# Kernel optimization log

Hardware: AMD Instinct MI355X
Metric: run time of the kernel (lower is better)

The kernel has to match this reference:

```python
import jax, jax.numpy as jnp
import numpy as np

N_NODES = 20000
N_EDGES = 200000
D_MODEL = 128
N_HEADS = 8
N_LAYERS = 2  # num_gnn - 1 concat layers


def setup_inputs() -> dict:
    key = jax.random.key(0)
    ks = jax.random.split(key, 12)
    s = 0.05  # keep activations well-scaled across residual layers
    hd = D_MODEL // N_HEADS  # 16
    return {
        "x": jax.random.normal(ks[0], (N_NODES, D_MODEL), jnp.float32),
        "src": jax.random.randint(ks[1], (N_EDGES,), 0, N_NODES),
        "dst": jax.random.randint(ks[2], (N_EDGES,), 0, N_NODES),
        "Ws": jax.random.normal(ks[3], (N_LAYERS, D_MODEL, D_MODEL), jnp.float32) * s,
        "als": jax.random.normal(ks[4], (N_LAYERS, N_HEADS, hd), jnp.float32) * s,
        "ars": jax.random.normal(ks[5], (N_LAYERS, N_HEADS, hd), jnp.float32) * s,
        "bs": jax.random.normal(ks[6], (N_LAYERS, D_MODEL), jnp.float32) * s,
        "W_last": jax.random.normal(ks[7], (D_MODEL, N_HEADS * D_MODEL), jnp.float32) * s,
        "al_last": jax.random.normal(ks[8], (N_HEADS, D_MODEL), jnp.float32) * s,
        "ar_last": jax.random.normal(ks[9], (N_HEADS, D_MODEL), jnp.float32) * s,
        "b_last": jax.random.normal(ks[10], (N_HEADS * D_MODEL,), jnp.float32) * s,
    }


def gat_conv(h, src, dst, W, al, ar, b, num_nodes):
    """DGL GATConv (eval mode, dropout off): returns (N, H, D) head outputs."""
    H, D = al.shape
    feat = (h @ W).reshape(num_nodes, H, D)          # (N,H,D)
    el = jnp.sum(feat * al[None], axis=-1)           # (N,H) attn on src side
    er = jnp.sum(feat * ar[None], axis=-1)           # (N,H) attn on dst side
    e = jax.nn.leaky_relu(el[src] + er[dst], 0.2)    # (E,H)
    # edge softmax over incoming edges of each dst node, per head
    m = jax.ops.segment_max(e, dst, num_segments=num_nodes)  # (N,H)
    p = jnp.exp(e - m[dst])                          # (E,H)
    z = jax.ops.segment_sum(p, dst, num_segments=num_nodes)  # (N,H)
    a = p / z[dst]                                   # (E,H)
    msg = feat[src] * a[..., None]                   # (E,H,D) weighted messages
    rst = jax.ops.segment_sum(msg, dst, num_segments=num_nodes)  # (N,H,D)
    return rst + b.reshape(1, H, D)


def reference(x, src, dst, Ws, als, ars, bs, W_last, al_last, ar_last, b_last):
    N = x.shape[0]
    h = x
    for i in range(N_LAYERS):
        temp = gat_conv(h, src, dst, Ws[i], als[i], ars[i], bs[i], N)  # (N,H,hd)
        h = h + jax.nn.elu(temp.reshape(N, -1))       # concat heads, ELU, residual
    temp = gat_conv(h, src, dst, W_last, al_last, ar_last, b_last, N)  # (N,H,D)
    h = h + jnp.mean(temp, axis=1)                    # mean over heads, residual
    return h
```

## Files before the change

kernel.cpp:

```cpp
#include <hip/hip_runtime.h>
#include <math.h>

#define N_NODES 20000
#define N_EDGES 200000
#define DM 128
#define NH 8

typedef __attribute__((ext_vector_type(8))) short bf16x8;
typedef __attribute__((ext_vector_type(4))) float f32x4;

__device__ __forceinline__ unsigned short f2b(float f) {
  unsigned int u = __float_as_uint(f);
  unsigned int r = (u + 0x7FFFu + ((u >> 16) & 1u)) >> 16;
  return (unsigned short)r;
}
__device__ __forceinline__ float b2f(unsigned short s) {
  return __uint_as_float(((unsigned int)s) << 16);
}

__global__ __launch_bounds__(256) void degzero(int* __restrict__ deg) {
  int i = blockIdx.x * 256 + threadIdx.x;
  if (i < N_NODES) deg[i] = 0;
}

__global__ __launch_bounds__(256) void prep_all(
    const float* __restrict__ x, float* __restrict__ h, unsigned short* __restrict__ hb,
    const int* __restrict__ dstE, int* __restrict__ deg, int* __restrict__ rank,
    const float* __restrict__ Ws, unsigned short* __restrict__ wsz,
    const float* __restrict__ W_last, unsigned short* __restrict__ wpsz,
    const float* __restrict__ al_last, const float* __restrict__ ar_last,
    const float* __restrict__ b_last, unsigned short* __restrict__ wlrsz,
    float* __restrict__ mb) {
  int i = blockIdx.x * 256 + threadIdx.x;
  if (i < (N_NODES * DM) / 4) {
    float4 v = ((const float4*)x)[i];
    ((float4*)h)[i] = v;
    ((ushort4*)hb)[i] = make_ushort4(f2b(v.x), f2b(v.y), f2b(v.z), f2b(v.w));
  }
  if (i < N_EDGES) rank[i] = atomicAdd(&deg[dstE[i]], 1);
  if (i < 2 * 16384) {
    int layer = i >> 14;
    int r = i & 16383;
    int j = r & 7, l = (r >> 3) & 63, f = (r >> 9) & 7, ks = r >> 12;
    int k = ks * 32 + ((l >> 4) << 3) + j;
    int n = f * 16 + (l & 15);
    wsz[i] = f2b(Ws[(size_t)layer * 16384 + k * 128 + n]);
  }
  if (i < 131072) {
    int j = i & 7, l = (i >> 3) & 63, f = (i >> 9) & 7, ks = i >> 12;
    int k = ks * 32 + ((l >> 4) << 3) + j;
    int n = f * 16 + (l & 15);
    int h_ = k >> 7, ko = k & 127;
    wpsz[i] = f2b(W_last[(size_t)ko * 1024 + h_ * 128 + n] * 0.125f);
  }
  if (i < 2048) {
    int j = i & 7, l = (i >> 3) & 63, ks = i >> 9;
    int k = ks * 32 + ((l >> 4) << 3) + j;
    int n = l & 15;
    int hh = n & 7;
    const float* av = (n < 8) ? (al_last + hh * 128) : (ar_last + hh * 128);
    float s = 0.f;
    for (int d = 0; d < 128; ++d) s += W_last[(size_t)k * 1024 + hh * 128 + d] * av[d];
    wlrsz[i] = f2b(s);
  }
  if (i < 128) {
    float s = 0.f;
#pragma unroll
    for (int hh = 0; hh < 8; ++hh) s += b_last[hh * 128 + i];
    mb[i] = s * 0.125f;
  }
}

__global__ void scan_deg(const int* __restrict__ deg, int* __restrict__ off,
                         int* __restrict__ bbase_g, int* __restrict__ bcur_g) {
  __shared__ int part[1024];
  __shared__ int hist[16][64];
  const int tid = threadIdx.x;
  const int wv = tid >> 6, lane = tid & 63;
  const int CHUNK = (N_NODES + 1023) / 1024;
  int base = tid * CHUNK;

  for (int i = tid; i < 16 * 64; i += 1024) ((int*)hist)[i] = 0;
  __syncthreads();

  int s = 0;
  for (int i = 0; i < CHUNK; ++i) {
    int idx = base + i;
    if (idx < N_NODES) {
      int d = deg[idx];
      s += d;
      atomicAdd(&hist[wv][min(d, 63)], 1);
    }
  }
  part[tid] = s;
  __syncthreads();
  for (int ofs = 1; ofs < 1024; ofs <<= 1) {
    int v = (tid >= ofs) ? part[tid - ofs] : 0;
    __syncthreads();
    part[tid] += v;
    __syncthreads();
  }
  int run = (tid > 0) ? part[tid - 1] : 0;
  for (int i = 0; i < CHUNK; ++i) {
    int idx = base + i;
    if (idx < N_NODES) {
      off[idx] = run;
      run += deg[idx];
    }
  }
  if (tid == 0) off[N_NODES] = part[1023];

  if (wv == 0) {
    int c = 0;
#pragma unroll
    for (int w = 0; w < 16; ++w) c += hist[w][lane];
    int inc = c;
#pragma unroll
    for (int ofs = 1; ofs < 64; ofs <<= 1) {
      int v = __shfl_up(inc, ofs, 64);
      if (lane >= ofs) inc += v;
    }
    bbase_g[lane] = inc - c;
    bcur_g[lane] = 0;
  }
}

template <int K>
__device__ __forceinline__ void dev_gemm(int tile, const unsigned short* __restrict__ A,
                                         const unsigned short* __restrict__ Bsz,
                                         unsigned short* __restrict__ Cb,
                                         const float* __restrict__ al,
                                         const float* __restrict__ ar,
                                         float* __restrict__ elr, int lane, int wid) {
  const int wrow = wid & 1, wc = wid >> 1;
  const int r0 = tile * 32;
  const int arow = r0 + wrow * 16 + (lane & 15);
  const int kg = lane >> 4;

  f32x4 acc[4];
#pragma unroll
  for (int fi = 0; fi < 4; ++fi) acc[fi] = {0.f, 0.f, 0.f, 0.f};

  const bf16x8* Ap = (const bf16x8*)(A + (size_t)arow * K + kg * 8);
#pragma unroll 4
  for (int ks = 0; ks < K / 32; ++ks) {
    bf16x8 a = Ap[ks * 4];
#pragma unroll
    for (int fi = 0; fi < 4; ++fi) {
      int f = wc * 4 + fi;
      bf16x8 b = *(const bf16x8*)(Bsz + (((size_t)(ks * 8 + f) * 64 + lane) << 3));
      acc[fi] = __builtin_amdgcn_mfma_f32_16x16x32_bf16(a, b, acc[fi], 0, 0, 0);
    }
  }

  const int rbase = r0 + wrow * 16 + (lane >> 4) * 4;
#pragma unroll
  for (int fi = 0; fi < 4; ++fi) {
    int col = wc * 64 + fi * 16 + (lane & 15);
#pragma unroll
    for (int r = 0; r < 4; ++r) {
      Cb[(size_t)(rbase + r) * DM + col] = f2b(acc[fi][r]);
    }
  }

#pragma unroll
  for (int fi = 0; fi < 4; ++fi) {
    int hh = wc * 4 + fi;
    float alv = al[hh * 16 + (lane & 15)];
    float arv = ar[hh * 16 + (lane & 15)];
#pragma unroll
    for (int r = 0; r < 4; ++r) {
      float pl = acc[fi][r] * alv;
      float pr = acc[fi][r] * arv;
#pragma unroll
      for (int msk = 1; msk < 16; msk <<= 1) {
        pl += __shfl_xor(pl, msk, 64);
        pr += __shfl_xor(pr, msk, 64);
      }
      if ((lane & 15) == 0) {
        int row = rbase + r;
        elr[row * 16 + hh] = pl;
        elr[row * 16 + 8 + hh] = pr;
      }
    }
  }
}

__global__ __launch_bounds__(256) void gemm0_scatter(
    const unsigned short* __restrict__ A, const unsigned short* __restrict__ Bsz,
    unsigned short* __restrict__ Cb, const float* __restrict__ al,
    const float* __restrict__ ar, float* __restrict__ elr, const int* __restrict__ srcE,
    const int* __restrict__ dstE, const int* __restrict__ rank,
    const int* __restrict__ off, int* __restrict__ csr_src, const int* __restrict__ deg,
    const int* __restrict__ bbase_g, int* __restrict__ bcur_g, int* __restrict__ perm) {
  __shared__ int lcnt[64];
  __shared__ int gbase[64];
  const int bid = blockIdx.x;
  const int GB = N_NODES / 32;
  const int EB = (N_EDGES + 255) / 256;
  if (bid < GB) {
    dev_gemm<DM>(bid, A, Bsz, Cb, al, ar, elr, threadIdx.x & 63, threadIdx.x >> 6);
  } else if (bid < GB + EB) {
    int e = (bid - GB) * 256 + threadIdx.x;
    if (e < N_EDGES) {
      csr_src[off[dstE[e]] + rank[e]] = srcE[e];
    }
  } else {
    const int tid = threadIdx.x;
    int idx = (bid - GB - EB) * 256 + tid;
    if (tid < 64) lcnt[tid] = 0;
    __syncthreads();
    int d = 0, lrank = 0;
    bool valid = idx < N_NODES;
    if (valid) {
      d = min(deg[idx], 63);
      lrank = atomicAdd(&lcnt[d], 1);
    }
    __syncthreads();
    if (tid < 64 && lcnt[tid] > 0) gbase[tid] = atomicAdd(&bcur_g[tid], lcnt[tid]);
    __syncthreads();
    if (valid) perm[bbase_g[d] + gbase[d] + lrank] = idx;
  }
}

template <int MODE>
__global__ __launch_bounds__(256) void fused_small(
    const int* __restrict__ perm, const int* __restrict__ off,
    const int* __restrict__ csr_src, const unsigned short* __restrict__ feat,
    const float* __restrict__ elr, const float* __restrict__ bias, float* __restrict__ h,
    unsigned short* __restrict__ hb, const unsigned short* __restrict__ wsz1,
    const float* __restrict__ al1, const float* __restrict__ ar1,
    unsigned short* __restrict__ feat_out, float* __restrict__ elr_out,
    const unsigned short* __restrict__ wlrsz, float* __restrict__ elr2_out) {
  __shared__ float a_lds[4][64];
  __shared__ int s_lds[4][8];
  __shared__ float zi_lds[4][8];
  __shared__ __align__(16) unsigned short nh_lds[4][128];
  __shared__ int pnode[4];
  const int wid = threadIdx.x >> 6;
  const int t = perm[blockIdx.x * 4 + wid];
  const int lane = threadIdx.x & 63;
  const int e_loc = lane >> 3, hh = lane & 7;
  const int hg = lane >> 3;
  const int beg = off[t], end = off[t + 1];
  const float ert = elr[t * 16 + 8 + hh];
  if (lane == 0) pnode[wid] = t;

  int e = beg + e_loc;
  bool val = e < end;
  int s = val ? csr_src[e] : 0;
  float xl = val ? elr[s * 16 + hh] : 0.f;

  float z = 0.f, acc0 = 0.f, acc1 = 0.f;
  for (int base = beg; base < end; base += 8) {
    float ex = 0.f;
    if (val) {
      float xv = xl + ert;
      xv = xv > 0.f ? xv : 0.2f * xv;
      ex = __expf(xv);
    }
    a_lds[wid][lane] = ex;
    if (hh == 0) s_lds[wid][e_loc] = s;
    __builtin_amdgcn_wave_barrier();
    asm volatile("s_waitcnt lgkmcnt(0)" ::: "memory");
    z += ex;
    int en = base + 8 + e_loc;
    bool valn = en < end;
    int sn = valn ? csr_src[en] : 0;
    float xln = valn ? elr[sn * 16 + hh] : 0.f;
    int n = min(8, end - base);
    if (n == 8) {
#pragma unroll
      for (int e2 = 0; e2 < 8; ++e2) {
        int s2 = s_lds[wid][e2];
        float a = a_lds[wid][e2 * 8 + hg];
        unsigned int hv = *(const unsigned int*)&feat[(size_t)s2 * 128 + 2 * lane];
        acc0 += a * b2f((unsigned short)(hv & 0xffffu));
        acc1 += a * b2f((unsigned short)(hv >> 16));
      }
    } else {
      for (int e2 = 0; e2 < n; ++e2) {
        int s2 = s_lds[wid][e2];
        float a = a_lds[wid][e2 * 8 + hg];
        unsigned int hv = *(const unsigned int*)&feat[(size_t)s2 * 128 + 2 * lane];
        acc0 += a * b2f((unsigned short)(hv & 0xffffu));
        acc1 += a * b2f((unsigned short)(hv >> 16));
      }
    }
    __builtin_amdgcn_wave_barrier();
    s = sn;
    xl = xln;
    val = valn;
  }
  z += __shfl_xor(z, 8, 64);
  z += __shfl_xor(z, 16, 64);
  z += __shfl_xor(z, 32, 64);
  if (e_loc == 0) zi_lds[wid][hh] = (z > 0.f) ? 1.f / z : 0.f;
  __builtin_amdgcn_wave_barrier();
  asm volatile("s_waitcnt lgkmcnt(0)" ::: "memory");
  float zi = zi_lds[wid][hg];

  float2 bv = *(const float2*)&bias[2 * lane];
  float v0 = acc0 * zi + bv.x;
  float v1 = acc1 * zi + bv.y;
  v0 = v0 > 0.f ? v0 : expm1f(v0);
  v1 = v1 > 0.f ? v1 : expm1f(v1);
  size_t idx = (size_t)t * 128 + 2 * lane;
  float2 hv = *(const float2*)&h[idx];
  float nh0 = hv.x + v0;
  float nh1 = hv.y + v1;
  *(float2*)&h[idx] = make_float2(nh0, nh1);
  unsigned short b0 = f2b(nh0), b1 = f2b(nh1);
  *(ushort2*)&hb[idx] = make_ushort2(b0, b1);
  *(ushort2*)&nh_lds[wid][2 * lane] = make_ushort2(b0, b1);

  if (MODE == 1) {
    __builtin_amdgcn_wave_barrier();
    asm volatile("s_waitcnt lgkmcnt(0)" ::: "memory");
    const int kg = lane >> 4;
    f32x4 acc = {0.f, 0.f, 0.f, 0.f};
#pragma unroll
    for (int ks = 0; ks < 4; ++ks) {
      bf16x8 a = *(const bf16x8*)&nh_lds[wid][ks * 32 + kg * 8];
      bf16x8 b = *(const bf16x8*)(wlrsz + (((size_t)ks * 64 + lane) << 3));
      acc = __builtin_amdgcn_mfma_f32_16x16x32_bf16(a, b, acc, 0, 0, 0);
    }
    if (lane < 16) elr2_out[t * 16 + lane] = acc[0];
  }

  if (MODE == 0) {
    __syncthreads();
    const int r16 = lane & 15;
    const int kg = lane >> 4;
    f32x4 acc2[2];
    acc2[0] = {0.f, 0.f, 0.f, 0.f};
    acc2[1] = {0.f, 0.f, 0.f, 0.f};
#pragma unroll
    for (int ks = 0; ks < 4; ++ks) {
      bf16x8 a = {0, 0, 0, 0, 0, 0, 0, 0};
      if (r16 < 4) a = *(const bf16x8*)&nh_lds[r16][ks * 32 + kg * 8];
#pragma unroll
      for (int fi = 0; fi < 2; ++fi) {
        int f = wid * 2 + fi;
        bf16x8 b = *(const bf16x8*)(wsz1 + (((size_t)(ks * 8 + f) * 64 + lane) << 3));
        acc2[fi] = __builtin_amdgcn_mfma_f32_16x16x32_bf16(a, b, acc2[fi], 0, 0, 0);
      }
    }
    const int rowl = (lane >> 4) * 4;
#pragma unroll
    for (int fi = 0; fi < 2; ++fi) {
      int f = wid * 2 + fi;
      int col = f * 16 + r16;
      float alv = al1[col];
      float arv = ar1[col];
#pragma unroll
      for (int r = 0; r < 4; ++r) {
        float v = acc2[fi][r];
        if (rowl == 0) feat_out[(size_t)pnode[r] * 128 + col] = f2b(v);
        float pl = v * alv;
        float pr = v * arv;
#pragma unroll
        for (int msk = 1; msk < 16; msk <<= 1) {
          pl += __shfl_xor(pl, msk, 64);
          pr += __shfl_xor(pr, msk, 64);
        }
        if (r16 == 0 && rowl == 0) {
          int pn = pnode[r];
          elr_out[pn * 16 + f] = pl;
          elr_out[pn * 16 + 8 + f] = pr;
        }
      }
    }
  }
}

#define GT_STRIDE 1032
__global__ __launch_bounds__(1024) void agg_gemm16(
    const int* __restrict__ perm, const int* __restrict__ off,
    const int* __restrict__ csr_src, const unsigned short* __restrict__ hb,
    const float* __restrict__ elr, const unsigned short* __restrict__ wpsz,
    const float* __restrict__ hres, const float* __restrict__ mb,
    float* __restrict__ out) {
  __shared__ __align__(16) unsigned short gt[16][GT_STRIDE];
  __shared__ float red[8][64][4];
  __shared__ float a_lds[16][64];
  __shared__ float zi_lds[16][8];
  __shared__ int pnode[16];
  const int wid = threadIdx.x >> 6;
  const int lane = threadIdx.x & 63;
  const int t0 = blockIdx.x * 16;
  const int t = perm[t0 + wid];
  const int e_loc = lane >> 3, hh = lane & 7;
  if (lane == 0) pnode[wid] = t;

  {
    const int beg = off[t], end = off[t + 1];
    const float ert = elr[t * 16 + 8 + hh];

    int eA = beg + e_loc;
    bool vA = eA < end;
    int sA = vA ? csr_src[eA] : 0;
    float xA = vA ? elr[sA * 16 + hh] : 0.f;
    int eB = beg + 8 + e_loc;
    bool vB = eB < end;
    int sB = vB ? csr_src[eB] : 0;
    float xB = vB ? elr[sB * 16 + hh] : 0.f;

    unsigned int hvc[8];
    {
      int n0 = end - beg;
      if (n0 > 8) n0 = 8;
#pragma unroll
      for (int e2 = 0; e2 < 8; ++e2) {
        if (e2 < n0) {
          int s2 = __shfl(sA, e2 * 8, 64);
          hvc[e2] = *(const unsigned int*)&hb[(size_t)s2 * 128 + 2 * lane];
        }
      }
    }

    float z = 0.f;
    float accA[8], accB[8];
#pragma unroll
    for (int k = 0; k < 8; ++k) accA[k] = accB[k] = 0.f;

    for (int base = beg; base < end; base += 8) {
      float ex = 0.f;
      if (vA) {
        float xv = xA + ert;
        xv = xv > 0.f ? xv : 0.2f * xv;
        ex = __expf(xv);
      }
      a_lds[wid][lane] = ex;
      __builtin_amdgcn_wave_barrier();
      asm volatile("s_waitcnt lgkmcnt(0)" ::: "memory");
      z += ex;

      unsigned int hvn[8];
      int n1 = end - base - 8;
      if (n1 > 8) n1 = 8;
#pragma unroll
      for (int e2 = 0; e2 < 8; ++e2) {
        if (e2 < n1) {
          int s2 = __shfl(sB, e2 * 8, 64);
          hvn[e2] = *(const unsigned int*)&hb[(size_t)s2 * 128 + 2 * lane];
        }
      }
      int eC = base + 16 + e_loc;
      bool vC = eC < end;
      int sC = vC ? csr_src[eC] : 0;
      float xC = vC ? elr[sC * 16 + hh] : 0.f;

      int n = end - base;
      if (n > 8) n = 8;
#pragma unroll
      for (int e2 = 0; e2 < 8; ++e2) {
        if (e2 < n) {
          float4 pa = *(const float4*)&a_lds[wid][e2 * 8];
          float4 pb = *(const float4*)&a_lds[wid][e2 * 8 + 4];
          float h0 = b2f((unsigned short)(hvc[e2] & 0xffffu));
          float h1 = b2f((unsigned short)(hvc[e2] >> 16));
          accA[0] += pa.x * h0; accB[0] += pa.x * h1;
          accA[1] += pa.y * h0; accB[1] += pa.y * h1;
          accA[2] += pa.z * h0; accB[2] += pa.z * h1;
          accA[3] += pa.w * h0; accB[3] += pa.w * h1;
          accA[4] += pb.x * h0; accB[4] += pb.x * h1;
          accA[5] += pb.y * h0; accB[5] += pb.y * h1;
          accA[6] += pb.z * h0; accB[6] += pb.z * h1;
          accA[7] += pb.w * h0; accB[7] += pb.w * h1;
        }
      }
      __builtin_amdgcn_wave_barrier();
#pragma unroll
      for (int e2 = 0; e2 < 8; ++e2) hvc[e2] = hvn[e2];
      sA = sB; xA = xB; vA = vB;
      sB = sC; xB = xC; vB = vC;
    }
    z += __shfl_xor(z, 8, 64);
    z += __shfl_xor(z, 16, 64);
    z += __shfl_xor(z, 32, 64);
    if (e_loc == 0) zi_lds[wid][hh] = (z > 0.f) ? 1.f / z : 0.f;
    __builtin_amdgcn_wave_barrier();
    asm volatile("s_waitcnt lgkmcnt(0)" ::: "memory");
    float4 zia = *(const float4*)&zi_lds[wid][0];
    float4 zib = *(const float4*)&zi_lds[wid][4];
    float ziv[8] = {zia.x, zia.y, zia.z, zia.w, zib.x, zib.y, zib.z, zib.w};
#pragma unroll
    for (int h2 = 0; h2 < 8; ++h2) {
      *(ushort2*)&gt[wid][h2 * 128 + 2 * lane] =
          make_ushort2(f2b(accA[h2] * ziv[h2]), f2b(accB[h2] * ziv[h2]));
    }
  }
  __syncthreads();

  const int f = wid & 7;
  const int kh = wid >> 3;
  const int ar16 = lane & 15;
  const int kg = lane >> 4;
  f32x4 acc = {0.f, 0.f, 0.f, 0.f};
#pragma unroll 4
  for (int ksl = 0; ksl < 16; ++ksl) {
    int ks = kh * 16 + ksl;
    bf16x8 a = *(const bf16x8*)&gt[ar16][ks * 32 + kg * 8];
    bf16x8 b = *(const bf16x8*)(wpsz + (((size_t)(ks * 8 + f) * 64 + lane) << 3));
    acc = __builtin_amdgcn_mfma_f32_16x16x32_bf16(a, b, acc, 0, 0, 0);
  }
  if (kh == 1) {
    *(float4*)&red[f][lane][0] = make_float4(acc[0], acc[1], acc[2], acc[3]);
  }
  __syncthreads();
  if (kh == 0) {
    float4 p = *(const float4*)&red[f][lane][0];
    const int col = f * 16 + (lane & 15);
    const int rb = (lane >> 4) * 4;
    float r4[4] = {p.x, p.y, p.z, p.w};
#pragma unroll
    for (int r = 0; r < 4; ++r) {
      int row = pnode[rb + r];
      out[(size_t)row * 128 + col] =
          acc[r] + r4[r] + hres[(size_t)row * 128 + col] + mb[col];
    }
  }
}

extern "C" void kernel_launch(void* const* d_in, const int* in_sizes, int n_in,
                              void* d_out, int out_size, void* d_ws, size_t ws_size,
                              hipStream_t stream) {
  const float* x = (const float*)d_in[0];
  const int* src = (const int*)d_in[1];
  const int* dst = (const int*)d_in[2];
  const float* Ws = (const float*)d_in[3];
  const float* als = (const float*)d_in[4];
  const float* ars = (const float*)d_in[5];
  const float* bs = (const float*)d_in[6];
  const float* W_last = (const float*)d_in[7];
  const float* al_last = (const float*)d_in[8];
  const float* ar_last = (const float*)d_in[9];
  const float* b_last = (const float*)d_in[10];
  float* out = (float*)d_out;

  float* h = (float*)d_ws;
  float* elr0 = h + 2560000;
  float* elrB = elr0 + 320000;
  float* elr2 = elrB + 320000;
  float* mb = elr2 + 320000;
  unsigned short* hb = (unsigned short*)(mb + 128);
  unsigned short* featA = hb + 2560000;
  unsigned short* featB = featA + 2560000;
  unsigned short* wsz = featB + 2560000;
  unsigned short* wpsz = wsz + 32768;
  unsigned short* wlrsz = wpsz + 131072;
  int* deg = (int*)(wlrsz + 2048);
  int* off = deg + N_NODES;
  int* rank = off + N_NODES + 1;
  int* csr_src = rank + N_EDGES;
  int* perm = csr_src + N_EDGES;
  int* bbase_g = perm + N_NODES;
  int* bcur_g = bbase_g + 64;

  const int GB = N_NODES / 32;
  const int FB = N_NODES / 4;
  const int EB = (N_EDGES + 255) / 256;
  const int PB = (N_NODES + 255) / 256;

  degzero<<<(N_NODES + 255) / 256, 256, 0, stream>>>(deg);
  prep_all<<<(N_NODES * DM / 4 + 255) / 256, 256, 0, stream>>>(
      x, h, hb, dst, deg, rank, Ws, wsz, W_last, wpsz, al_last, ar_last, b_last, wlrsz, mb);
  scan_deg<<<1, 1024, 0, stream>>>(deg, off, bbase_g, bcur_g);
  gemm0_scatter<<<GB + EB + PB, 256, 0, stream>>>(hb, wsz, featA, als, ars, elr0, src,
                                                  dst, rank, off, csr_src, deg, bbase_g,
                                                  bcur_g, perm);
  fused_small<0><<<FB, 256, 0, stream>>>(perm, off, csr_src, featA, elr0, bs, h, hb,
                                         wsz + 16384, als + 128, ars + 128, featB, elrB,
                                         nullptr, nullptr);
  fused_small<1><<<FB, 256, 0, stream>>>(perm, off, csr_src, featB, elrB, bs + 128, h, hb,
                                         nullptr, nullptr, nullptr, nullptr, nullptr,
                                         wlrsz, elr2);
  agg_gemm16<<<N_NODES / 16, 1024, 0, stream>>>(perm, off, csr_src, hb, elr2, wpsz, h, mb,
                                                out);
}
```

Baseline: 164.5 us.

## Software-pipeline neighbor feature gathers one batch ahead in fused_small

The edge loop of fused_small now keeps the gathered bf16 feature rows for the next 8-edge batch in registers, issuing those loads before consuming the current batch. Edge indices and attention logits are prefetched two batches ahead. Source indices are broadcast with __shfl instead of staging them through LDS. The aim is to hide gather latency behind the accumulation math, at the cost of more registers (two 8-entry buffers) and possible occupancy loss.

```diff
diff --git a/kernel.cpp b/kernel.cpp
--- a/kernel.cpp
+++ b/kernel.cpp
@@ -233,7 +233,6 @@
     unsigned short* __restrict__ feat_out, float* __restrict__ elr_out,
     const unsigned short* __restrict__ wlrsz, float* __restrict__ elr2_out) {
   __shared__ float a_lds[4][64];
-  __shared__ int s_lds[4][8];
   __shared__ float zi_lds[4][8];
   __shared__ __align__(16) unsigned short nh_lds[4][128];
   __shared__ int pnode[4];
@@ -246,51 +245,71 @@
   const float ert = elr[t * 16 + 8 + hh];
   if (lane == 0) pnode[wid] = t;
 
-  int e = beg + e_loc;
-  bool val = e < end;
-  int s = val ? csr_src[e] : 0;
-  float xl = val ? elr[s * 16 + hh] : 0.f;
+  int eA = beg + e_loc;
+  bool vA = eA < end;
+  int sA = vA ? csr_src[eA] : 0;
+  float xA = vA ? elr[sA * 16 + hh] : 0.f;
+  int eB = beg + 8 + e_loc;
+  bool vB = eB < end;
+  int sB = vB ? csr_src[eB] : 0;
+  float xB = vB ? elr[sB * 16 + hh] : 0.f;
+
+  unsigned int hvc[8];
+  {
+    int n0 = end - beg;
+    if (n0 > 8) n0 = 8;
+#pragma unroll
+    for (int e2 = 0; e2 < 8; ++e2) {
+      if (e2 < n0) {
+        int s2 = __shfl(sA, e2 * 8, 64);
+        hvc[e2] = *(const unsigned int*)&feat[(size_t)s2 * 128 + 2 * lane];
+      }
+    }
+  }
 
   float z = 0.f, acc0 = 0.f, acc1 = 0.f;
   for (int base = beg; base < end; base += 8) {
     float ex = 0.f;
-    if (val) {
-      float xv = xl + ert;
+    if (vA) {
+      float xv = xA + ert;
       xv = xv > 0.f ? xv : 0.2f * xv;
       ex = __expf(xv);
     }
     a_lds[wid][lane] = ex;
-    if (hh == 0) s_lds[wid][e_loc] = s;
     __builtin_amdgcn_wave_barrier();
     asm volatile("s_waitcnt lgkmcnt(0)" ::: "memory");
     z += ex;
-    int en = base + 8 + e_loc;
-    bool valn = en < end;
-    int sn = valn ? csr_src[en] : 0;
-    float xln = valn ? elr[sn * 16 + hh] : 0.f;
-    int n = min(8, end - base);
-    if (n == 8) {
-#pragma unroll
-      for (int e2 = 0; e2 < 8; ++e2) {
-        int s2 = s_lds[wid][e2];
+
+    unsigned int hvn[8];
+    int n1 = end - base - 8;
+    if (n1 > 8) n1 = 8;
+#pragma unroll
+    for (int e2 = 0; e2 < 8; ++e2) {
+      if (e2 < n1) {
+        int s2 = __shfl(sB, e2 * 8, 64);
+        hvn[e2] = *(const unsigned int*)&feat[(size_t)s2 * 128 + 2 * lane];
+      }
+    }
+    int eC = base + 16 + e_loc;
+    bool vC = eC < end;
+    int sC = vC ? csr_src[eC] : 0;
+    float xC = vC ? elr[sC * 16 + hh] : 0.f;
+
+    int n = end - base;
+    if (n > 8) n = 8;
+#pragma unroll
+    for (int e2 = 0; e2 < 8; ++e2) {
+      if (e2 < n) {
         float a = a_lds[wid][e2 * 8 + hg];
-        unsigned int hv = *(const unsigned int*)&feat[(size_t)s2 * 128 + 2 * lane];
-        acc0 += a * b2f((unsigned short)(hv & 0xffffu));
-        acc1 += a * b2f((unsigned short)(hv >> 16));
-      }
-    } else {
-      for (int e2 = 0; e2 < n; ++e2) {
-        int s2 = s_lds[wid][e2];
-        float a = a_lds[wid][e2 * 8 + hg];
-        unsigned int hv = *(const unsigned int*)&feat[(size_t)s2 * 128 + 2 * lane];
-        acc0 += a * b2f((unsigned short)(hv & 0xffffu));
-        acc1 += a * b2f((unsigned short)(hv >> 16));
+        acc0 += a * b2f((unsigned short)(hvc[e2] & 0xffffu));
+        acc1 += a * b2f((unsigned short)(hvc[e2] >> 16));
       }
     }
     __builtin_amdgcn_wave_barrier();
-    s = sn;
-    xl = xln;
-    val = valn;
+#pragma unroll
+    for (int e2 = 0; e2 < 8; ++e2) hvc[e2] = hvn[e2];
+    sA = sB; xA = xB; vA = vB;
+    sB = sC; xB = xC; vB = vC;
   }
   z += __shfl_xor(z, 8, 64);
   z += __shfl_xor(z, 16, 64);
```

Measured after the change: 172.4 us. 1.05x slower.
